# Kernel tuning notes

Measured on AMD Instinct MI355X. Metric: run time of the kernel, lower is better.

## Reference

```python
import jax, jax.numpy as jnp
import numpy as np

DIM = 512
NUM_GROUPS = 32
EPS = 1e-6
INV_SQRT2 = 0.7071067811865476


def group_norm(x, gamma, beta):
    # x: [b, c, h, w]; GroupNorm with NUM_GROUPS groups, per-channel affine
    b, c, h, w = x.shape
    xg = x.reshape(b, NUM_GROUPS, c // NUM_GROUPS, h, w)
    mu = xg.mean(axis=(2, 3, 4), keepdims=True)
    var = xg.var(axis=(2, 3, 4), keepdims=True)
    xn = ((xg - mu) * jax.lax.rsqrt(var + EPS)).reshape(b, c, h, w)
    return xn * gamma[None, :, None, None] + beta[None, :, None, None]


def conv1x1(x, w, b):
    # 1x1 conv == per-pixel GEMM over channels. w: [out_c, in_c], b: [out_c]
    return jnp.einsum('oc,bchw->bohw', w, x) + b[None, :, None, None]


def setup_inputs() -> dict:
    key = jax.random.key(0)
    ks = jax.random.split(key, 6)
    b, c, h, w = 4, DIM, 64, 64
    q = jax.random.normal(ks[0], (b, c, h, w), dtype=jnp.float32)
    init = lambda k: jax.random.normal(k, (DIM, DIM), dtype=jnp.float32) * 0.02
    return {
        'q': q,
        'gamma': jnp.ones((DIM,), jnp.float32),
        'beta': jnp.zeros((DIM,), jnp.float32),
        'wq': init(ks[1]), 'bq': jnp.zeros((DIM,), jnp.float32),
        'wk': init(ks[2]), 'bk': jnp.zeros((DIM,), jnp.float32),
        'wv': init(ks[3]), 'bv': jnp.zeros((DIM,), jnp.float32),
        'wo': init(ks[4]), 'bo': jnp.zeros((DIM,), jnp.float32),
    }


def reference(q, gamma, beta, wq, bq, wk, bk, wv, bv, wo, bo):
    q_in = q
    x = group_norm(q, gamma, beta)  # self-attention path: v is None -> v = normed q
    qp = conv1x1(x, wq, bq)
    kp = conv1x1(x, wk, bk)
    vp = conv1x1(x, wv, bv)
    b, c, h, w = qp.shape
    qf = qp.reshape(b, c, h * w)
    kf = kp.reshape(b, c, h * w)
    vf = vp.reshape(b, c, h * w)
    # scores[b, i, j] = sum_c k[b,c,i] * q[b,c,j]; softmax over i (key axis, dim=-2)
    scores = jnp.einsum('bci,bcj->bij', kf, qf) * (c ** -0.5)
    attn = jax.nn.softmax(scores, axis=-2)
    out = jnp.einsum('bci,bij->bcj', vf, attn).reshape(b, c, h, w)
    out = conv1x1(out, wo, bo)
    return (out + q_in) * INV_SQRT2
```

## Files before the change

kernel.cpp:

```cpp
#include <hip/hip_runtime.h>

typedef __bf16 bf16;
typedef __bf16 bf16x8 __attribute__((ext_vector_type(8)));
typedef float floatx4 __attribute__((ext_vector_type(4)));

#define SCALE_QK 0.044194173824159216f
#define INV_SQRT2F 0.7071067811865476f
#define TEN  8388608L
#define SBAT 2097152L
#define SPB  16777216L

typedef const __attribute__((address_space(1))) void GV;
typedef __attribute__((address_space(3))) void SV;

__global__ __launch_bounds__(256) void detect_k(
    const unsigned* __restrict__ q, int* __restrict__ flag)
{
    __shared__ int cnt;
    if (threadIdx.x == 0) cnt = 0;
    __syncthreads();
    int c = 0;
    for (int i = threadIdx.x; i < 4096; i += 256) {
        unsigned e = (q[i] >> 7) & 0xFFu;
        c += (e >= 100u && e <= 140u) ? 1 : 0;
    }
    atomicAdd(&cnt, c);
    __syncthreads();
    if (threadIdx.x == 0) *flag = (cnt < 3000) ? 1 : 0;
}

__global__ __launch_bounds__(256) void zero_k(float* __restrict__ l)
{
    for (int i = threadIdx.x; i < 16384; i += 256) l[i] = 0.f;
}

__global__ __launch_bounds__(256) void convw_k(
    const void* w0, const void* w1, const void* w2, const void* w3,
    bf16* __restrict__ dst, const int* __restrict__ flag)
{
    const void* srcs[4] = {w0, w1, w2, w3};
    const void* s = srcs[blockIdx.y];
    bf16* d = dst + (size_t)blockIdx.y * 262144;
    const int i = (blockIdx.x * 256 + threadIdx.x) * 8;
    bf16x8 v;
    if (*flag) {
        const float* f = (const float*)s;
        #pragma unroll
        for (int r = 0; r < 8; ++r) v[r] = (bf16)f[i + r];
    } else {
        v = *(const bf16x8*)((const bf16*)s + i);
    }
    *(bf16x8*)(d + i) = v;
}

__global__ __launch_bounds__(256) void convp_k(
    const void* p0, const void* p1, const void* p2,
    const void* p3, const void* p4, const void* p5,
    float* __restrict__ dst, const int* __restrict__ flag)
{
    const void* srcs[6] = {p0, p1, p2, p3, p4, p5};
    const int f = *flag;
    for (int i = threadIdx.x; i < 3072; i += 256) {
        const void* s = srcs[i >> 9];
        const int off = i & 511;
        dst[i] = f ? ((const float*)s)[off] : (float)((const bf16*)s)[off];
    }
}

__global__ __launch_bounds__(256) void groupnorm_k(
    const void* __restrict__ qraw, const float* __restrict__ gamma,
    const float* __restrict__ beta, bf16* __restrict__ XN,
    const int* __restrict__ flag)
{
    const int tid = threadIdx.x;
    const int b = blockIdx.x >> 5, g = blockIdx.x & 31;
    const int f32 = *flag;
    const size_t base = ((size_t)b * 512 + (size_t)g * 16) * 4096;
    const float* sf = (const float*)qraw + base;
    const bf16*  sb = (const bf16*)qraw + base;

    float sum = 0.f, sq = 0.f;
    if (f32) {
        const floatx4* v4 = (const floatx4*)sf;
        for (int idx = tid; idx < 16384; idx += 256) {
            floatx4 v = v4[idx];
            #pragma unroll
            for (int r = 0; r < 4; ++r) { float f = v[r]; sum += f; sq += f * f; }
        }
    } else {
        const bf16x8* v8 = (const bf16x8*)sb;
        for (int idx = tid; idx < 8192; idx += 256) {
            bf16x8 v = v8[idx];
            #pragma unroll
            for (int r = 0; r < 8; ++r) { float f = (float)v[r]; sum += f; sq += f * f; }
        }
    }
    #pragma unroll
    for (int off = 32; off; off >>= 1) {
        sum += __shfl_down(sum, off);
        sq  += __shfl_down(sq, off);
    }
    __shared__ float sS[4], sQ[4];
    __shared__ float s_mean, s_rstd;
    const int wave = tid >> 6, lane = tid & 63;
    if (lane == 0) { sS[wave] = sum; sQ[wave] = sq; }
    __syncthreads();
    if (tid == 0) {
        float ts = sS[0] + sS[1] + sS[2] + sS[3];
        float tq = sQ[0] + sQ[1] + sQ[2] + sQ[3];
        float mean = ts * (1.0f / 65536.0f);
        float var  = tq * (1.0f / 65536.0f) - mean * mean;
        s_mean = mean;
        s_rstd = rsqrtf(fmaxf(var, 0.f) + 1e-6f);
    }
    __syncthreads();
    const float mean = s_mean, rstd = s_rstd;

    float ga[16], be[16];
    #pragma unroll
    for (int c = 0; c < 16; ++c) {
        ga[c] = gamma[g * 16 + c] * rstd;
        be[c] = beta[g * 16 + c] - mean * ga[c];
    }
    bf16* dst = XN + (size_t)b * SBAT + (size_t)g * 16;
    for (int p0 = 0; p0 < 4096; p0 += 256) {
        const int p = p0 + tid;
        bf16x8 o0, o1;
        #pragma unroll
        for (int c = 0; c < 8; ++c) {
            float v = f32 ? sf[(size_t)c * 4096 + p] : (float)sb[(size_t)c * 4096 + p];
            o0[c] = (bf16)(v * ga[c] + be[c]);
        }
        #pragma unroll
        for (int c = 0; c < 8; ++c) {
            float v = f32 ? sf[(size_t)(c + 8) * 4096 + p] : (float)sb[(size_t)(c + 8) * 4096 + p];
            o1[c] = (bf16)(v * ga[c + 8] + be[c + 8]);
        }
        bf16* dp = dst + (size_t)p * 512;
        *(bf16x8*)dp = o0;
        *(bf16x8*)(dp + 8) = o1;
    }
}

__global__ __launch_bounds__(256) void reduce_k(
    const bf16* __restrict__ Part, const float* __restrict__ lbuf,
    bf16* __restrict__ AOt)
{
    const size_t i8 = ((size_t)blockIdx.x * 256 + threadIdx.x) * 8;
    const int b = (int)(i8 >> 21);
    const int j = (int)((i8 >> 9) & 4095);
    const float rl = 1.0f / fmaxf(lbuf[b * 4096 + j], 1e-30f);
    bf16x8 a = *(const bf16x8*)&Part[i8];
    bf16x8 c = *(const bf16x8*)&Part[TEN + i8];
    bf16x8 o;
    #pragma unroll
    for (int r = 0; r < 8; ++r) o[r] = (bf16)(((float)a[r] + (float)c[r]) * rl);
    *(bf16x8*)&AOt[i8] = o;
}

template <int EPI>
__global__ __launch_bounds__(256, 4) void gemm_xyt(
    const bf16* __restrict__ Xb, const bf16* __restrict__ Yb,
    void* __restrict__ Cv, int N, int K, int lda, int ldb,
    long sX, long sY, long sC,
    const float* __restrict__ bias,
    float* __restrict__ lbuf, long sL,
    const void* __restrict__ res, long sR,
    const int* __restrict__ flag)
{
    __shared__ __align__(16) bf16 smem[17408];

    const int tid  = threadIdx.x;
    const int wave = tid >> 6;
    const int lane = tid & 63;
    const int z = blockIdx.z;

    int bx = blockIdx.x, by = blockIdx.y;
    {
        const int gx = gridDim.x, gy = gridDim.y;
        const int o = by * gx + bx;
        const int xcd = o & 7, idx = o >> 3;
        if (gx == 32 && gy == 32) {
            bx = (xcd & 1) * 16 + (idx & 15);
            by = (xcd >> 1) * 8 + (idx >> 4);
        } else if (gx == 4) {
            bx = idx & 3;
            by = xcd * 4 + (idx >> 2);
        } else if (gx == 32 && gy == 4) {
            bx = (xcd & 1) * 16 + (idx & 15);
            by = xcd >> 1;
        }
    }

    const bf16* X; const bf16* Y; bf16* Cb; float* Cf = nullptr;
    int zb = z;
    if (EPI == 5) {
        const int b = z >> 1, s = z & 1;
        X  = Xb + (size_t)b * SPB  + (size_t)s * 2048;
        Y  = Yb + (size_t)b * SBAT + (size_t)s * 2048;
        Cb = (bf16*)Cv + (size_t)s * TEN + (size_t)b * SBAT;
        zb = b;
    } else {
        X  = Xb + (long)z * sX;
        Y  = Yb + (long)z * sY;
        Cb = (bf16*)Cv  + (long)z * sC;
        Cf = (float*)Cv + (long)z * sC;
    }
    const int f32o = (EPI == 4) ? *flag : 0;

    const int m0 = by * 128, n0 = bx * 128;
    const int wm = (wave >> 1) * 64, wn = (wave & 1) * 64;
    const int fr = lane & 15, quad = lane >> 4;

    const int srow = tid >> 2;
    const int scol = (tid & 3) * 8;
    const bf16* pX = X + (size_t)(m0 + srow) * lda + scol;
    const bf16* pY = Y + (size_t)(n0 + srow) * ldb + scol;
    const size_t oX = (size_t)64 * lda, oY = (size_t)64 * ldb;
    char* const sb0 = (char*)smem;
    const int ldst = tid * 16;

    auto stage = [&](int k, int pb) {
        char* d = sb0 + pb * 16384;
        const bf16* x = pX + k * 32;
        const bf16* y = pY + k * 32;
        __builtin_amdgcn_global_load_lds((GV*)x,        (SV*)(d + ldst),         16, 0, 0);
        __builtin_amdgcn_global_load_lds((GV*)(x + oX), (SV*)(d + 4096 + ldst),  16, 0, 0);
        __builtin_amdgcn_global_load_lds((GV*)y,        (SV*)(d + 8192 + ldst),  16, 0, 0);
        __builtin_amdgcn_global_load_lds((GV*)(y + oY), (SV*)(d + 12288 + ldst), 16, 0, 0);
    };

    floatx4 acc[4][4] = {};
    const int NK = K >> 5;

    stage(0, 0);
    __syncthreads();

    for (int k = 0; k < NK; ++k) {
        const int p = k & 1;
        if (k + 1 < NK) stage(k + 1, 1 - p);
        const bf16* bA = smem + p * 8192;
        const bf16* bB = bA + 4096;
        bf16x8 af[4], bfr[4];
        #pragma unroll
        for (int i = 0; i < 4; ++i) {
            af[i]  = *(const bf16x8*)&bA[(wm + i * 16 + fr) * 32 + quad * 8];
            bfr[i] = *(const bf16x8*)&bB[(wn + i * 16 + fr) * 32 + quad * 8];
        }
        #pragma unroll
        for (int i = 0; i < 4; ++i)
            #pragma unroll
            for (int j = 0; j < 4; ++j)
                acc[i][j] = __builtin_amdgcn_mfma_f32_16x16x32_bf16(
                    af[i], bfr[j], acc[i][j], 0, 0, 0);
        __syncthreads();
    }

    #pragma unroll
    for (int i = 0; i < 4; ++i) {
        const int mg = m0 + wm + i * 16 + quad * 4;
        float bmr[4], rl[4];
        if (EPI == 1 || EPI == 4) {
            #pragma unroll
            for (int r = 0; r < 4; ++r) bmr[r] = bias[mg + r];
        }
        if (EPI == 3) {
            #pragma unroll
            for (int r = 0; r < 4; ++r)
                rl[r] = 1.0f / fmaxf(lbuf[zb * sL + mg + r], 1e-30f);
        }
        if (EPI == 2) {
            float rs[4] = {0.f, 0.f, 0.f, 0.f};
            #pragma unroll
            for (int j = 0; j < 4; ++j)
                #pragma unroll
                for (int r = 0; r < 4; ++r) {
                    float e = __expf(fminf(acc[i][j][r] * SCALE_QK, 30.f));
                    acc[i][j][r] = e;
                    rs[r] += e;
                }
            #pragma unroll
            for (int r = 0; r < 4; ++r) {
                float v = rs[r];
                v += __shfl_xor(v, 1);
                v += __shfl_xor(v, 2);
                v += __shfl_xor(v, 4);
                v += __shfl_xor(v, 8);
                if (fr == 0) atomicAdd(&lbuf[zb * sL + mg + r], v);
            }
        } else if (EPI != 5) {
            #pragma unroll
            for (int j = 0; j < 4; ++j) {
                const int ng = n0 + wn + j * 16 + fr;
                #pragma unroll
                for (int r = 0; r < 4; ++r) {
                    float v = acc[i][j][r];
                    if (EPI == 0) v += bias[ng];
                    if (EPI == 1) v += bmr[r];
                    if (EPI == 3) v *= rl[r];
                    if (EPI == 4) v += bmr[r];
                    acc[i][j][r] = v;
                }
            }
        }
    }

    if (EPI != 4) {
        bf16* ct = smem;
        #pragma unroll
        for (int i = 0; i < 4; ++i)
            #pragma unroll
            for (int j = 0; j < 4; ++j)
                #pragma unroll
                for (int r = 0; r < 4; ++r)
                    ct[(wm + i * 16 + quad * 4 + r) * 132 + wn + j * 16 + fr] =
                        (bf16)acc[i][j][r];
        __syncthreads();
        #pragma unroll
        for (int w = 0; w < 8; ++w) {
            const int idx = w * 2048 + tid * 8;
            const int row = idx >> 7, col = idx & 127;
            bf16x8 v = *(const bf16x8*)&ct[row * 132 + col];
            *(bf16x8*)&Cb[(size_t)(m0 + row) * N + n0 + col] = v;
        }
    } else if (f32o) {
        float* ct = (float*)smem;
        const float* rres = (const float*)res + (size_t)z * sR;
        #pragma unroll
        for (int h = 0; h < 2; ++h) {
            if ((wave >> 1) == h) {
                #pragma unroll
                for (int i = 0; i < 4; ++i)
                    #pragma unroll
                    for (int j = 0; j < 4; ++j)
                        #pragma unroll
                        for (int r = 0; r < 4; ++r)
                            ct[(i * 16 + quad * 4 + r) * 132 + wn + j * 16 + fr] =
                                acc[i][j][r];
            }
            __syncthreads();
            #pragma unroll
            for (int w = 0; w < 8; ++w) {
                const int idx = (w * 256 + tid) * 4;
                const int row = idx >> 7, col = idx & 127;
                const size_t o = (size_t)(m0 + h * 64 + row) * N + n0 + col;
                floatx4 v = *(const floatx4*)&ct[row * 132 + col];
                floatx4 rv = *(const floatx4*)&rres[o];
                #pragma unroll
                for (int e = 0; e < 4; ++e) v[e] = (v[e] + rv[e]) * INV_SQRT2F;
                *(floatx4*)&Cf[o] = v;
            }
            __syncthreads();
        }
    } else {
        const bf16* resb = (const bf16*)res + (size_t)z * sR;
        #pragma unroll
        for (int i = 0; i < 4; ++i) {
            const int mg = m0 + wm + i * 16 + quad * 4;
            #pragma unroll
            for (int j = 0; j < 4; ++j) {
                const int ng = n0 + wn + j * 16 + fr;
                #pragma unroll
                for (int r = 0; r < 4; ++r) {
                    const size_t o = (size_t)(mg + r) * N + ng;
                    Cb[o] = (bf16)((acc[i][j][r] + (float)resb[o]) * INV_SQRT2F);
                }
            }
        }
    }
}

extern "C" void kernel_launch(void* const* d_in, const int* in_sizes, int n_in,
                              void* d_out, int out_size, void* d_ws, size_t ws_size,
                              hipStream_t stream)
{
    const void* q     = d_in[0];
    const void* gamma = d_in[1];
    const void* beta  = d_in[2];
    const void* wq    = d_in[3];
    const void* bq    = d_in[4];
    const void* wk    = d_in[5];
    const void* bk    = d_in[6];
    const void* wv    = d_in[7];
    const void* bv    = d_in[8];
    const void* wo    = d_in[9];
    const void* bo    = d_in[10];

    char* w = (char*)d_ws;
    int*   flag = (int*)w;   w += 16;
    float* Pf   = (float*)w; w += 6 * 512 * 4;
    bf16*  Wc   = (bf16*)w;  w += 4 * 262144 * 2;
    bf16*  XN   = (bf16*)w;  w += TEN * 2;
    bf16*  Qt   = (bf16*)w;  w += TEN * 2;
    bf16*  V    = (bf16*)w;  w += TEN * 2;
    float* lbuf = (float*)w; w += (size_t)4 * 4096 * 4;
    bf16*  P    = (bf16*)w;
    const size_t base_need = (size_t)(w - (char*)d_ws);
    const bool full = ws_size >= base_need + (size_t)4 * 4096 * 4096 * 2;

    bf16* Kt   = (bf16*)d_out;
    bf16* Part = (bf16*)d_out;
    bf16* AOt  = XN;

    detect_k<<<dim3(1), 256, 0, stream>>>((const unsigned*)q, flag);
    zero_k<<<dim3(1), 256, 0, stream>>>(lbuf);
    convw_k<<<dim3(128, 4), 256, 0, stream>>>(wq, wk, wv, wo, Wc, flag);
    convp_k<<<dim3(1), 256, 0, stream>>>(gamma, beta, bq, bk, bv, bo, Pf, flag);

    groupnorm_k<<<dim3(128), 256, 0, stream>>>(q, Pf, Pf + 512, XN, flag);

    gemm_xyt<0><<<dim3(4, 32, 4), 256, 0, stream>>>(XN, Wc + 0 * 262144, Qt,
        512, 512, 512, 512, SBAT, 0, SBAT, Pf + 1024, nullptr, 0, nullptr, 0, flag);
    gemm_xyt<0><<<dim3(4, 32, 4), 256, 0, stream>>>(XN, Wc + 1 * 262144, Kt,
        512, 512, 512, 512, SBAT, 0, SBAT, Pf + 1536, nullptr, 0, nullptr, 0, flag);
    gemm_xyt<1><<<dim3(32, 4, 4), 256, 0, stream>>>(Wc + 2 * 262144, XN, V,
        4096, 512, 512, 512, 0, SBAT, SBAT, Pf + 2048, nullptr, 0, nullptr, 0, flag);

    if (full) {
        gemm_xyt<2><<<dim3(32, 32, 4), 256, 0, stream>>>(Qt, Kt, P,
            4096, 512, 512, 512, SBAT, SBAT, SPB, nullptr, lbuf, 4096,
            nullptr, 0, flag);
        gemm_xyt<5><<<dim3(4, 32, 8), 256, 0, stream>>>(P, V, Part,
            512, 2048, 4096, 4096, 0, 0, 0, nullptr, nullptr, 0,
            nullptr, 0, flag);
        reduce_k<<<dim3(4096), 256, 0, stream>>>(Part, lbuf, AOt);
    } else {
        for (int b = 0; b < 4; ++b) {
            gemm_xyt<2><<<dim3(32, 32, 1), 256, 0, stream>>>(
                Qt + (size_t)b * SBAT, Kt + (size_t)b * SBAT, P,
                4096, 512, 512, 512, 0, 0, 0, nullptr,
                lbuf + (size_t)b * 4096, 0, nullptr, 0, flag);
            gemm_xyt<3><<<dim3(4, 32, 1), 256, 0, stream>>>(
                P, V + (size_t)b * SBAT, AOt + (size_t)b * SBAT,
                512, 4096, 4096, 4096, 0, 0, 0, nullptr,
                lbuf + (size_t)b * 4096, 0, nullptr, 0, flag);
        }
    }

    gemm_xyt<4><<<dim3(32, 4, 4), 256, 0, stream>>>(Wc + 3 * 262144, AOt, d_out,
        4096, 512, 512, 512, 0, SBAT, SBAT, Pf + 2560, nullptr, 0, q, SBAT, flag);
}
```

Baseline: 515.9 us.

## Fuse QK^T, softmax and PV into a single flash-style attention kernel

Replaces the materialized 4096x4096 score matrix (QK GEMM with atomic row sums, split PV GEMM, reduce kernel) with one fused attention kernel. Each 512-thread block keeps its Q tile in registers, streams K and V tiles through swizzled LDS via direct global-to-LDS loads, exponentiates scores into an LDS P tile and accumulates P·V with 32x32 MFMAs, normalizing at the end. Q and K projections are merged into one GEMM writing an interleaved QKt buffer. This removes the large P write/read traffic and the atomics, at the cost of 144KB LDS per block, only 256 blocks, and no running-max rescaling (relies on the clamp at 30, as the old code did).

```diff
diff --git a/kernel.cpp b/kernel.cpp
--- a/kernel.cpp
+++ b/kernel.cpp
@@ -3,12 +3,12 @@
 typedef __bf16 bf16;
 typedef __bf16 bf16x8 __attribute__((ext_vector_type(8)));
 typedef float floatx4 __attribute__((ext_vector_type(4)));
+typedef float floatx16 __attribute__((ext_vector_type(16)));
 
 #define SCALE_QK 0.044194173824159216f
 #define INV_SQRT2F 0.7071067811865476f
 #define TEN  8388608L
 #define SBAT 2097152L
-#define SPB  16777216L
 
 typedef const __attribute__((address_space(1))) void GV;
 typedef __attribute__((address_space(3))) void SV;
@@ -27,11 +27,6 @@
     atomicAdd(&cnt, c);
     __syncthreads();
     if (threadIdx.x == 0) *flag = (cnt < 3000) ? 1 : 0;
-}
-
-__global__ __launch_bounds__(256) void zero_k(float* __restrict__ l)
-{
-    for (int i = threadIdx.x; i < 16384; i += 256) l[i] = 0.f;
 }
 
 __global__ __launch_bounds__(256) void convw_k(
@@ -142,20 +137,169 @@
     }
 }
 
-__global__ __launch_bounds__(256) void reduce_k(
-    const bf16* __restrict__ Part, const float* __restrict__ lbuf,
+__global__ __launch_bounds__(512, 2) void fused_attn(
+    const bf16* __restrict__ QKt,
+    const bf16* __restrict__ V,
     bf16* __restrict__ AOt)
 {
-    const size_t i8 = ((size_t)blockIdx.x * 256 + threadIdx.x) * 8;
-    const int b = (int)(i8 >> 21);
-    const int j = (int)((i8 >> 9) & 4095);
-    const float rl = 1.0f / fmaxf(lbuf[b * 4096 + j], 1e-30f);
-    bf16x8 a = *(const bf16x8*)&Part[i8];
-    bf16x8 c = *(const bf16x8*)&Part[TEN + i8];
-    bf16x8 o;
+    __shared__ __align__(16) char smc[147456];
+
+    const int tid = threadIdx.x;
+    const int w = tid >> 6, lane = tid & 63;
+    const int fr = lane & 15, quad = lane >> 4;
+    const int l5 = lane >> 5, l31 = lane & 31;
+
+    const int ll = blockIdx.x;
+    const int xcd = ll & 7, rr = ll >> 3;
+    const int b = xcd >> 1;
+    const int mtile = (xcd & 1) * 32 + rr;
+    const int j0 = mtile * 64;
+
+    const bf16* Qb = QKt + (size_t)b * 4194304;
+    const bf16* Kb = Qb + 512;
+    const bf16* Vb = V + (size_t)b * SBAT;
+
+    const int wmQ = (w >> 1) * 16;
+    const int wnQ = (w & 1) * 64;
+    bf16x8 qf[16];
+    {
+        const bf16* qsrc = Qb + (size_t)(j0 + wmQ + fr) * 1024 + quad * 8;
+        #pragma unroll
+        for (int s = 0; s < 16; ++s) qf[s] = *(const bf16x8*)(qsrc + s * 32);
+    }
+
+    const int lcK = ((tid & 15) ^ ((tid >> 4) & 7)) << 3;
+    const int rowK = tid >> 4;
+    auto stageK = [&](int key0, int kd0, int buf) {
+        char* d = smc + buf * 32768;
+        const bf16* s0 = Kb + (size_t)(key0 + rowK) * 1024 + kd0 + lcK;
+        #pragma unroll
+        for (int rho = 0; rho < 4; ++rho)
+            __builtin_amdgcn_global_load_lds((GV*)(s0 + (size_t)rho * 32 * 1024),
+                (SV*)(d + rho * 8192 + tid * 16), 16, 0, 0);
+    };
+    const int lcV = ((tid & 3) ^ ((tid >> 3) & 3)) << 3;
+    const int rowV = tid >> 2;
+    auto stageV = [&](int i0, int buf) {
+        char* d = smc + 65536 + buf * 32768;
+        const bf16* s0 = Vb + (size_t)rowV * 4096 + i0 + lcV;
+        #pragma unroll
+        for (int rho = 0; rho < 4; ++rho)
+            __builtin_amdgcn_global_load_lds((GV*)(s0 + (size_t)rho * 128 * 4096),
+                (SV*)(d + rho * 8192 + tid * 16), 16, 0, 0);
+    };
+
+    const int wmP = (w >> 2) * 32;
+    const int wnP = (w & 3) * 128;
+
+    floatx16 acc_o[4] = {};
+    float l_acc[4] = {};
+
+    const int swzQK = (fr & 7) << 4;
+    const int prow = wmP + l31;
+    const int swzP = (prow & 7) << 4;
+
+    stageK(0, 0, 0);
+    __syncthreads();
+
+    for (int c = 0; c < 32; ++c) {
+        const int k0 = c * 128;
+        floatx4 acc_s[4] = {};
+
+        #pragma unroll
+        for (int s = 0; s < 4; ++s) {
+            if (s < 3)      stageK(k0, (s + 1) * 128, (s + 1) & 1);
+            else            stageV(k0, 0);
+            const char* kb = smc + (s & 1) * 32768;
+            #pragma unroll
+            for (int ks = 0; ks < 4; ++ks) {
+                #pragma unroll
+                for (int nf = 0; nf < 4; ++nf) {
+                    const int key = wnQ + nf * 16 + fr;
+                    bf16x8 bf8 = *(const bf16x8*)(kb + key * 256 +
+                        ((ks * 64 + quad * 16) ^ swzQK));
+                    acc_s[nf] = __builtin_amdgcn_mfma_f32_16x16x32_bf16(
+                        qf[s * 4 + ks], bf8, acc_s[nf], 0, 0, 0);
+                }
+            }
+            __syncthreads();
+        }
+
+        {
+            float rs[4] = {0.f, 0.f, 0.f, 0.f};
+            #pragma unroll
+            for (int nf = 0; nf < 4; ++nf) {
+                const int i = wnQ + nf * 16 + fr;
+                #pragma unroll
+                for (int r = 0; r < 4; ++r) {
+                    const int j = wmQ + quad * 4 + r;
+                    float e = __expf(fminf(acc_s[nf][r] * SCALE_QK, 30.f));
+                    rs[r] += e;
+                    *(bf16*)(smc + 131072 + j * 256 +
+                             ((i * 2) ^ ((j & 7) << 4))) = (bf16)e;
+                }
+            }
+            #pragma unroll
+            for (int r = 0; r < 4; ++r) {
+                float v = rs[r];
+                v += __shfl_xor(v, 1);
+                v += __shfl_xor(v, 2);
+                v += __shfl_xor(v, 4);
+                v += __shfl_xor(v, 8);
+                l_acc[r] += v;
+            }
+        }
+        __syncthreads();
+
+        #pragma unroll
+        for (int sv = 0; sv < 4; ++sv) {
+            if (sv < 3)          stageV(k0 + (sv + 1) * 32, (sv + 1) & 1);
+            else if (c < 31)     stageK(k0 + 128, 0, 0);
+            const char* vb = smc + 65536 + (sv & 1) * 32768;
+            const char* pb = smc + 131072;
+            #pragma unroll
+            for (int ih = 0; ih < 2; ++ih) {
+                const int is = sv * 2 + ih;
+                bf16x8 pa = *(const bf16x8*)(pb + prow * 256 +
+                    ((is * 32 + l5 * 16) ^ swzP));
+                #pragma unroll
+                for (int nf = 0; nf < 4; ++nf) {
+                    const int cc = wnP + nf * 32 + l31;
+                    bf16x8 vb8 = *(const bf16x8*)(vb + cc * 64 +
+                        ((ih * 32 + l5 * 16) ^ (((cc >> 1) & 3) << 4)));
+                    acc_o[nf] = __builtin_amdgcn_mfma_f32_32x32x16_bf16(
+                        pa, vb8, acc_o[nf], 0, 0, 0);
+                }
+            }
+            __syncthreads();
+        }
+    }
+
+    float* lsh = (float*)smc;
+    if (fr == 0) {
+        #pragma unroll
+        for (int r = 0; r < 4; ++r) lsh[w * 16 + quad * 4 + r] = l_acc[r];
+    }
+    __syncthreads();
+    float* rsh = (float*)(smc + 512);
+    if (tid < 64) {
+        const int wp = (tid >> 4) << 1;
+        rsh[tid] = 1.0f / fmaxf(lsh[wp * 16 + (tid & 15)] +
+                                lsh[(wp + 1) * 16 + (tid & 15)], 1e-30f);
+    }
+    __syncthreads();
+
+    bf16* out = AOt + (size_t)b * SBAT + (size_t)j0 * 512;
     #pragma unroll
-    for (int r = 0; r < 8; ++r) o[r] = (bf16)(((float)a[r] + (float)c[r]) * rl);
-    *(bf16x8*)&AOt[i8] = o;
+    for (int reg = 0; reg < 16; ++reg) {
+        const int j = wmP + (reg & 3) + 8 * (reg >> 2) + 4 * l5;
+        const float rl = rsh[j];
+        #pragma unroll
+        for (int nf = 0; nf < 4; ++nf) {
+            const int cc = wnP + nf * 32 + l31;
+            out[(size_t)j * 512 + cc] = (bf16)(acc_o[nf][reg] * rl);
+        }
+    }
 }
 
 template <int EPI>
@@ -164,7 +308,6 @@
     void* __restrict__ Cv, int N, int K, int lda, int ldb,
     long sX, long sY, long sC,
     const float* __restrict__ bias,
-    float* __restrict__ lbuf, long sL,
     const void* __restrict__ res, long sR,
     const int* __restrict__ flag)
 {
@@ -180,32 +323,19 @@
         const int gx = gridDim.x, gy = gridDim.y;
         const int o = by * gx + bx;
         const int xcd = o & 7, idx = o >> 3;
-        if (gx == 32 && gy == 32) {
-            bx = (xcd & 1) * 16 + (idx & 15);
-            by = (xcd >> 1) * 8 + (idx >> 4);
-        } else if (gx == 4) {
-            bx = idx & 3;
-            by = xcd * 4 + (idx >> 2);
+        if (gx == 8) {
+            bx = xcd;
+            by = idx;
         } else if (gx == 32 && gy == 4) {
             bx = (xcd & 1) * 16 + (idx & 15);
             by = xcd >> 1;
         }
     }
 
-    const bf16* X; const bf16* Y; bf16* Cb; float* Cf = nullptr;
-    int zb = z;
-    if (EPI == 5) {
-        const int b = z >> 1, s = z & 1;
-        X  = Xb + (size_t)b * SPB  + (size_t)s * 2048;
-        Y  = Yb + (size_t)b * SBAT + (size_t)s * 2048;
-        Cb = (bf16*)Cv + (size_t)s * TEN + (size_t)b * SBAT;
-        zb = b;
-    } else {
-        X  = Xb + (long)z * sX;
-        Y  = Yb + (long)z * sY;
-        Cb = (bf16*)Cv  + (long)z * sC;
-        Cf = (float*)Cv + (long)z * sC;
-    }
+    const bf16* X = Xb + (long)z * sX;
+    const bf16* Y = Yb + (long)z * sY;
+    bf16*  Cb = (bf16*)Cv  + (long)z * sC;
+    float* Cf = (float*)Cv + (long)z * sC;
     const int f32o = (EPI == 4) ? *flag : 0;
 
     const int m0 = by * 128, n0 = bx * 128;
@@ -259,48 +389,21 @@
     #pragma unroll
     for (int i = 0; i < 4; ++i) {
         const int mg = m0 + wm + i * 16 + quad * 4;
-        float bmr[4], rl[4];
+        float bmr[4];
         if (EPI == 1 || EPI == 4) {
             #pragma unroll
             for (int r = 0; r < 4; ++r) bmr[r] = bias[mg + r];
         }
-        if (EPI == 3) {
-            #pragma unroll
-            for (int r = 0; r < 4; ++r)
-                rl[r] = 1.0f / fmaxf(lbuf[zb * sL + mg + r], 1e-30f);
-        }
-        if (EPI == 2) {
-            float rs[4] = {0.f, 0.f, 0.f, 0.f};
-            #pragma unroll
-            for (int j = 0; j < 4; ++j)
-                #pragma unroll
-                for (int r = 0; r < 4; ++r) {
-                    float e = __expf(fminf(acc[i][j][r] * SCALE_QK, 30.f));
-                    acc[i][j][r] = e;
-                    rs[r] += e;
-                }
+        #pragma unroll
+        for (int j = 0; j < 4; ++j) {
+            const int ng = n0 + wn + j * 16 + fr;
             #pragma unroll
             for (int r = 0; r < 4; ++r) {
-                float v = rs[r];
-                v += __shfl_xor(v, 1);
-                v += __shfl_xor(v, 2);
-                v += __shfl_xor(v, 4);
-                v += __shfl_xor(v, 8);
-                if (fr == 0) atomicAdd(&lbuf[zb * sL + mg + r], v);
-            }
-        } else if (EPI != 5) {
-            #pragma unroll
-            for (int j = 0; j < 4; ++j) {
-                const int ng = n0 + wn + j * 16 + fr;
-                #pragma unroll
-                for (int r = 0; r < 4; ++r) {
-                    float v = acc[i][j][r];
-                    if (EPI == 0) v += bias[ng];
-                    if (EPI == 1) v += bmr[r];
-                    if (EPI == 3) v *= rl[r];
-                    if (EPI == 4) v += bmr[r];
-                    acc[i][j][r] = v;
-                }
+                float v = acc[i][j][r];
+                if (EPI == 0) v += bias[ng];
+                if (EPI == 1) v += bmr[r];
+                if (EPI == 4) v += bmr[r];
+                acc[i][j][r] = v;
             }
         }
     }
@@ -391,52 +494,26 @@
     float* Pf   = (float*)w; w += 6 * 512 * 4;
     bf16*  Wc   = (bf16*)w;  w += 4 * 262144 * 2;
     bf16*  XN   = (bf16*)w;  w += TEN * 2;
-    bf16*  Qt   = (bf16*)w;  w += TEN * 2;
+    bf16*  QKt  = (bf16*)w;  w += (size_t)4 * 4096 * 1024 * 2;
     bf16*  V    = (bf16*)w;  w += TEN * 2;
-    float* lbuf = (float*)w; w += (size_t)4 * 4096 * 4;
-    bf16*  P    = (bf16*)w;
-    const size_t base_need = (size_t)(w - (char*)d_ws);
-    const bool full = ws_size >= base_need + (size_t)4 * 4096 * 4096 * 2;
-
-    bf16* Kt   = (bf16*)d_out;
-    bf16* Part = (bf16*)d_out;
-    bf16* AOt  = XN;
+    bf16*  AOt  = XN;
 
     detect_k<<<dim3(1), 256, 0, stream>>>((const unsigned*)q, flag);
-    zero_k<<<dim3(1), 256, 0, stream>>>(lbuf);
     convw_k<<<dim3(128, 4), 256, 0, stream>>>(wq, wk, wv, wo, Wc, flag);
     convp_k<<<dim3(1), 256, 0, stream>>>(gamma, beta, bq, bk, bv, bo, Pf, flag);
 
     groupnorm_k<<<dim3(128), 256, 0, stream>>>(q, Pf, Pf + 512, XN, flag);
 
-    gemm_xyt<0><<<dim3(4, 32, 4), 256, 0, stream>>>(XN, Wc + 0 * 262144, Qt,
-        512, 512, 512, 512, SBAT, 0, SBAT, Pf + 1024, nullptr, 0, nullptr, 0, flag);
-    gemm_xyt<0><<<dim3(4, 32, 4), 256, 0, stream>>>(XN, Wc + 1 * 262144, Kt,
-        512, 512, 512, 512, SBAT, 0, SBAT, Pf + 1536, nullptr, 0, nullptr, 0, flag);
+    gemm_xyt<0><<<dim3(8, 32, 4), 256, 0, stream>>>(XN, Wc, QKt,
+        1024, 512, 512, 512, SBAT, 0, (long)4096 * 1024, Pf + 1024,
+        nullptr, 0, flag);
     gemm_xyt<1><<<dim3(32, 4, 4), 256, 0, stream>>>(Wc + 2 * 262144, XN, V,
-        4096, 512, 512, 512, 0, SBAT, SBAT, Pf + 2048, nullptr, 0, nullptr, 0, flag);
-
-    if (full) {
-        gemm_xyt<2><<<dim3(32, 32, 4), 256, 0, stream>>>(Qt, Kt, P,
-            4096, 512, 512, 512, SBAT, SBAT, SPB, nullptr, lbuf, 4096,
-            nullptr, 0, flag);
-        gemm_xyt<5><<<dim3(4, 32, 8), 256, 0, stream>>>(P, V, Part,
-            512, 2048, 4096, 4096, 0, 0, 0, nullptr, nullptr, 0,
-            nullptr, 0, flag);
-        reduce_k<<<dim3(4096), 256, 0, stream>>>(Part, lbuf, AOt);
-    } else {
-        for (int b = 0; b < 4; ++b) {
-            gemm_xyt<2><<<dim3(32, 32, 1), 256, 0, stream>>>(
-                Qt + (size_t)b * SBAT, Kt + (size_t)b * SBAT, P,
-                4096, 512, 512, 512, 0, 0, 0, nullptr,
-                lbuf + (size_t)b * 4096, 0, nullptr, 0, flag);
-            gemm_xyt<3><<<dim3(4, 32, 1), 256, 0, stream>>>(
-                P, V + (size_t)b * SBAT, AOt + (size_t)b * SBAT,
-                512, 4096, 4096, 4096, 0, 0, 0, nullptr,
-                lbuf + (size_t)b * 4096, 0, nullptr, 0, flag);
-        }
-    }
+        4096, 512, 512, 512, 0, SBAT, SBAT, Pf + 2048,
+        nullptr, 0, flag);
+
+    fused_attn<<<dim3(256), 512, 0, stream>>>(QKt, V, AOt);
 
     gemm_xyt<4><<<dim3(32, 4, 4), 256, 0, stream>>>(Wc + 3 * 262144, AOt, d_out,
-        4096, 512, 512, 512, 0, SBAT, SBAT, Pf + 2560, nullptr, 0, q, SBAT, flag);
-}
+        4096, 512, 512, 512, 0, SBAT, SBAT, Pf + 2560,
+        q, SBAT, flag);
+}
```

Result: faster. 505.2 us (-2.1%).
